# Optimization experiments

Measured on AMD Instinct MI355X. Metric: run time of the kernel, lower is better.

Reference implementation:

```python
import jax, jax.numpy as jnp
import numpy as np

B, N, F_IN, F_E, H, L = 8, 128, 64, 16, 256, 8
EPS = 1e-5


def _linear_params(key, fan_in, fan_out):
    k1, k2 = jax.random.split(key)
    bound = 1.0 / np.sqrt(fan_in)
    W = jax.random.uniform(k1, (fan_in, fan_out), minval=-bound, maxval=bound, dtype=jnp.float32)
    b = jax.random.uniform(k2, (fan_out,), minval=-bound, maxval=bound, dtype=jnp.float32)
    return W, b


def setup_inputs() -> dict:
    key = jax.random.key(0)
    ks = jax.random.split(key, 16)
    x = jax.random.normal(ks[0], (B, N, F_IN), dtype=jnp.float32)
    adj = jax.random.randint(ks[1], (B, N, N), 0, 2, dtype=jnp.int32)
    edge_attr = jax.random.normal(ks[2], (B, N, N, F_E), dtype=jnp.float32)
    mask = jnp.ones((B, N), dtype=jnp.int32)

    node_W, node_b = _linear_params(ks[3], F_IN, H)
    edge_W, edge_b = _linear_params(ks[4], F_E, H)

    lks = jax.random.split(ks[5], L)
    W1s, b1s, W2s, b2s = [], [], [], []
    for i in range(L):
        a, b_ = jax.random.split(lks[i])
        W1, b1 = _linear_params(a, H, H)
        W2, b2 = _linear_params(b_, H, H)
        W1s.append(W1); b1s.append(b1); W2s.append(W2); b2s.append(b2)
    ln_g = jnp.ones((L, H), dtype=jnp.float32)
    ln_b = jnp.zeros((L, H), dtype=jnp.float32)
    W1 = jnp.stack(W1s); b1 = jnp.stack(b1s)
    W2 = jnp.stack(W2s); b2 = jnp.stack(b2s)

    ro_pW, ro_pb = _linear_params(ks[6], H, H)
    ro_aW, ro_ab = _linear_params(ks[7], H, 1)
    ph_W, ph_b = _linear_params(ks[8], H, 1)

    return dict(x=x, adj=adj, edge_attr=edge_attr, mask=mask,
                node_W=node_W, node_b=node_b, edge_W=edge_W, edge_b=edge_b,
                ln_g=ln_g, ln_b=ln_b, W1=W1, b1=b1, W2=W2, b2=b2,
                ro_pW=ro_pW, ro_pb=ro_pb, ro_aW=ro_aW, ro_ab=ro_ab,
                ph_W=ph_W, ph_b=ph_b)


def _layernorm(x, g, b):
    mu = jnp.mean(x, axis=-1, keepdims=True)
    var = jnp.var(x, axis=-1, keepdims=True)
    return (x - mu) * jax.lax.rsqrt(var + EPS) * g + b


def _gine_forward(x, adjf, edge_attr, maskf,
                  node_W, node_b, edge_W, edge_b,
                  ln_g, ln_b, W1, b1, W2, b2,
                  ro_pW, ro_pb, ro_aW, ro_ab, ph_W, ph_b):
    h = x @ node_W + node_b                      # (B,N,H)
    edge_emb = edge_attr @ edge_W + edge_b       # (B,N,N,H)
    m = maskf[..., None]                         # (B,N,1)

    def layer(h, p):
        g, bln, w1, bb1, w2, bb2 = p
        h = h * m
        h_norm = _layernorm(h, g, bln)
        # message: h_j + e_ij, j indexes axis 2 -> broadcast over axis 1
        m_in = h_norm[:, None, :, :] + edge_emb          # (B,N,N,H)
        mm = jax.nn.relu(jax.nn.relu(m_in @ w1 + bb1) @ w2 + bb2)
        mm = mm * adjf[..., None]
        msg = mm.sum(axis=2)                             # (B,N,H)
        out = (h + msg) * m
        return out, None

    h, _ = jax.lax.scan(layer, h, (ln_g, ln_b, W1, b1, W2, b2))

    # attention readout
    hp = jnp.tanh(h @ ro_pW + ro_pb)
    scores = (hp @ ro_aW).squeeze(-1) + ro_ab            # (B,N)
    scores = jnp.where(maskf > 0, scores, -jnp.inf)
    alpha = jax.nn.softmax(scores, axis=1)
    cnt = jnp.clip(maskf.sum(axis=1, keepdims=True), 1.0, None)
    fallback = jnp.where(maskf > 0, 1.0 / cnt, 0.0)
    alpha = jnp.where(jnp.isnan(alpha), fallback, alpha)
    gvec = (h * alpha[..., None]).sum(axis=1)            # (B,H)
    out = (gvec @ ph_W + ph_b).squeeze(-1)               # (B,)
    return out


def reference(x, adj, edge_attr, mask,
              node_W, node_b, edge_W, edge_b,
              ln_g, ln_b, W1, b1, W2, b2,
              ro_pW, ro_pb, ro_aW, ro_ab, ph_W, ph_b):
    adjf = adj.astype(jnp.float32)
    maskf = mask.astype(jnp.float32)
    return _gine_forward(x, adjf, edge_attr, maskf,
                         node_W, node_b, edge_W, edge_b,
                         ln_g, ln_b, W1, b1, W2, b2,
                         ro_pW, ro_pb, ro_aW, ro_ab, ph_W, ph_b)
```

## Files before the change

kernel.cpp:

```cpp
#include <hip/hip_runtime.h>

typedef float  f32x4   __attribute__((ext_vector_type(4)));
typedef short  bf16x8  __attribute__((ext_vector_type(8)));
typedef unsigned short u16;
typedef unsigned int   u32;

static __device__ __forceinline__ u16 f2bf(float f) {
    u32 u = __float_as_uint(f);
    u += 0x7FFFu + ((u >> 16) & 1u);
    return (u16)(u >> 16);
}



__global__ void k_h0ln(const float* __restrict__ x, const float* __restrict__ nW,
                       const float* __restrict__ nb, const int* __restrict__ mask,
                       const float* __restrict__ lng, const float* __restrict__ lnb,
                       float* __restrict__ h, u16* __restrict__ hnbf) {
    __shared__ float xr[64];
    __shared__ float rs[4], rs2[4];
    int row = blockIdx.x, c = threadIdx.x;
    if (c < 64) xr[c] = x[row * 64 + c];
    __syncthreads();
    float acc = nb[c];
#pragma unroll
    for (int k = 0; k < 64; ++k) acc += xr[k] * nW[k * 256 + c];
    float mv = (float)mask[row];
    float v = acc * mv;
    h[row * 256 + c] = v;
    float s = v, s2 = v * v;
    int w = c >> 6, lane = c & 63;
#pragma unroll
    for (int off = 32; off; off >>= 1) {
        s  += __shfl_xor(s,  off);
        s2 += __shfl_xor(s2, off);
    }
    if (lane == 0) { rs[w] = s; rs2[w] = s2; }
    __syncthreads();
    float S  = rs[0] + rs[1] + rs[2] + rs[3];
    float S2 = rs2[0] + rs2[1] + rs2[2] + rs2[3];
    float mu  = S * (1.f / 256.f);
    float var = S2 * (1.f / 256.f) - mu * mu;
    float rstd = rsqrtf(var + 1e-5f);
    hnbf[row * 256 + c] = f2bf((v - mu) * rstd * lng[c] + lnb[c]);
}

__global__ void k_edgefrag(const float* __restrict__ ea, u16* __restrict__ ef) {
    int gid = blockIdx.x * 256 + threadIdx.x;
    int lane = gid & 63, nt = (gid >> 6) & 7, i = (gid >> 9) & 127, b = gid >> 16;
    int j = nt * 16 + (lane & 15), k0 = (lane >> 4) * 8;
    uint4 out = {0u, 0u, 0u, 0u};
    if (k0 < 16) {
        const float* p = ea + (((size_t)(b * 128 + i) * 128 + j) * 16 + k0);
        u16 us[8];
#pragma unroll
        for (int t = 0; t < 8; ++t) us[t] = f2bf(p[t]);
        out.x = (u32)us[0] | ((u32)us[1] << 16);
        out.y = (u32)us[2] | ((u32)us[3] << 16);
        out.z = (u32)us[4] | ((u32)us[5] << 16);
        out.w = (u32)us[6] | ((u32)us[7] << 16);
    }
    ((uint4*)ef)[gid] = out;
}

__global__ void k_wt(const float* __restrict__ W1, const float* __restrict__ W2,
                     u16* __restrict__ w1t, u16* __restrict__ w2t) {
    int gid = blockIdx.x * 256 + threadIdx.x;
    int lane = gid & 63, mt = (gid >> 6) & 15, kt = (gid >> 10) & 7, l = gid >> 13;
    int hh = mt * 16 + (lane & 15), k = kt * 32 + (lane >> 4) * 8;
    u16 a[8], b[8];
#pragma unroll
    for (int t = 0; t < 8; ++t) {
        size_t idx = (size_t)l * 65536 + (size_t)(k + t) * 256 + hh;
        a[t] = f2bf(W1[idx]);
        b[t] = f2bf(W2[idx]);
    }
    uint4 oa, ob;
    oa.x = (u32)a[0] | ((u32)a[1] << 16); oa.y = (u32)a[2] | ((u32)a[3] << 16);
    oa.z = (u32)a[4] | ((u32)a[5] << 16); oa.w = (u32)a[6] | ((u32)a[7] << 16);
    ob.x = (u32)b[0] | ((u32)b[1] << 16); ob.y = (u32)b[2] | ((u32)b[3] << 16);
    ob.z = (u32)b[4] | ((u32)b[5] << 16); ob.w = (u32)b[6] | ((u32)b[7] << 16);
    ((uint4*)w1t)[gid] = oa;
    ((uint4*)w2t)[gid] = ob;
}

__global__ void k_pwt(const float* __restrict__ pW, u16* __restrict__ pwt) {
    int gid = blockIdx.x * 256 + threadIdx.x;
    int lane = gid & 63, mt = (gid >> 6) & 15, kt = gid >> 10;
    int hh = mt * 16 + (lane & 15), k = kt * 32 + (lane >> 4) * 8;
    u16 a[8];
#pragma unroll
    for (int t = 0; t < 8; ++t) a[t] = f2bf(pW[(size_t)(k + t) * 256 + hh]);
    uint4 o;
    o.x = (u32)a[0] | ((u32)a[1] << 16); o.y = (u32)a[2] | ((u32)a[3] << 16);
    o.z = (u32)a[4] | ((u32)a[5] << 16); o.w = (u32)a[6] | ((u32)a[7] << 16);
    ((uint4*)pwt)[gid] = o;
}

__global__ void k_wf1b(const float* __restrict__ eW, const float* __restrict__ eb,
                       const float* __restrict__ W1, const float* __restrict__ b1,
                       u16* __restrict__ wf, float* __restrict__ bias1) {
    __shared__ float eWsT[256 * 16];
    __shared__ float ebS[256];
    int l = blockIdx.x, tid = threadIdx.x;
#pragma unroll
    for (int k = 0; k < 16; ++k) eWsT[tid * 16 + k] = eW[k * 256 + tid];
    ebS[tid] = eb[tid];
    __syncthreads();
    float acc[16];
#pragma unroll
    for (int k = 0; k < 16; ++k) acc[k] = 0.f;
    float bacc = b1[l * 256 + tid];
    const float* w1c = W1 + (size_t)l * 65536 + tid;
    for (int c = 0; c < 256; ++c) {
        float wv = w1c[(size_t)c * 256];
        const f32x4* e = (const f32x4*)&eWsT[c * 16];
#pragma unroll
        for (int q = 0; q < 4; ++q) {
            f32x4 ev = e[q];
#pragma unroll
            for (int t = 0; t < 4; ++t) acc[q * 4 + t] += ev[t] * wv;
        }
        bacc += ebS[c] * wv;
    }
    bias1[l * 256 + tid] = bacc;
    int mt = tid >> 4, lo = tid & 15;
#pragma unroll
    for (int c4 = 0; c4 < 4; ++c4) {
        u16 us[8];
#pragma unroll
        for (int t = 0; t < 8; ++t) {
            int k = c4 * 8 + t;
            us[t] = (k < 16) ? f2bf(acc[k]) : (u16)0;
        }
        uint4 o;
        o.x = (u32)us[0] | ((u32)us[1] << 16);
        o.y = (u32)us[2] | ((u32)us[3] << 16);
        o.z = (u32)us[4] | ((u32)us[5] << 16);
        o.w = (u32)us[6] | ((u32)us[7] << 16);
        ((uint4*)wf)[(size_t)(l * 16 + mt) * 64 + c4 * 16 + lo] = o;
    }
}


__global__ __launch_bounds__(256) void k_hn1(const u16* __restrict__ w1t,
        const u16* __restrict__ hnbf, const float* __restrict__ bias1,
        float* __restrict__ hn1p, int l) {
    int orig = blockIdx.x;
    int bid = (orig & 7) * 16 + (orig >> 3);
    int b = bid >> 4, mt = bid & 15;
    int tid = threadIdx.x, w = tid >> 6, lane = tid & 63;
    f32x4 bv = *(const f32x4*)(bias1 + l * 256 + mt * 16 + (lane >> 4) * 4);
    f32x4 acc0 = bv, acc1 = bv;
    int j0 = (w * 2) * 16 + (lane & 15), j1 = j0 + 16;
#pragma unroll
    for (int kt = 0; kt < 8; ++kt) {
        bf16x8 a = *(const bf16x8*)(w1t + ((size_t)((l * 8 + kt) * 16 + mt) * 64 + lane) * 8);
        bf16x8 bt0 = *(const bf16x8*)(hnbf + ((size_t)(b * 128 + j0) * 256 + kt * 32 + (lane >> 4) * 8));
        bf16x8 bt1 = *(const bf16x8*)(hnbf + ((size_t)(b * 128 + j1) * 256 + kt * 32 + (lane >> 4) * 8));
        acc0 = __builtin_amdgcn_mfma_f32_16x16x32_bf16(a, bt0, acc0, 0, 0, 0);
        acc1 = __builtin_amdgcn_mfma_f32_16x16x32_bf16(a, bt1, acc1, 0, 0, 0);
    }
    float* outb = hn1p + (size_t)b * 32768;
    *(f32x4*)(outb + ((size_t)(mt * 8 + w * 2) * 64 + lane) * 4)     = acc0;
    *(f32x4*)(outb + ((size_t)(mt * 8 + w * 2 + 1) * 64 + lane) * 4) = acc1;
}

__global__ __launch_bounds__(512, 4) void k_msg(
        const u16* __restrict__ wf1t, const u16* __restrict__ ef,
        const u16* __restrict__ w2t,  const float* __restrict__ hn1p,
        const float* __restrict__ b2, const int* __restrict__ adj,
        const int* __restrict__ mask, float* __restrict__ h,
        const float* __restrict__ lngN, const float* __restrict__ lnbN,
        u16* __restrict__ hnbf, int l, int doLN) {

    __shared__ __align__(16) u16  t1S[8 * 8 * 64 * 8];
    __shared__ __align__(16) float b2S[256];
    __shared__ __align__(16) float msgS[256];
    __shared__ int rankS[128];
    __shared__ int cntS;
    __shared__ float rs[8], rs2[8];

    int orig = blockIdx.x;
    int bid = (orig & 7) * 128 + (orig >> 3);
    int b = bid >> 7, i = bid & 127;
    int tid = threadIdx.x, w = tid >> 6, lane = tid & 63;
    int row = b * 128 + i;

    if (tid < 256) b2S[tid] = b2[l * 256 + tid];
    if (w == 0) {
        int f0 = adj[(size_t)row * 128 + lane] != 0;
        int f1 = adj[(size_t)row * 128 + 64 + lane] != 0;
        unsigned long long m0 = __ballot(f0);
        unsigned long long m1 = __ballot(f1);
        unsigned long long lt = (1ull << lane) - 1ull;
        int c0 = __popcll(m0);
        rankS[lane]      = f0 ? __popcll(m0 & lt)      : -1;
        rankS[64 + lane] = f1 ? c0 + __popcll(m1 & lt) : -1;
        if (lane == 0) cntS = c0 + __popcll(m1);
    }
    __syncthreads();
    int cnt = cntS;
    int NT = (cnt + 15) >> 4;

    {
        int c = cnt + (lane >> 2);
        int kg = lane & 3;
        if (c < NT * 16) {
            uint4 z = {0u, 0u, 0u, 0u};
            *(uint4*)(t1S + ((size_t)((w * 8 + (c >> 4)) * 64 + kg * 16 + (c & 15)) * 8)) = z;
        }
    }

    const u16*  efb = ef + (size_t)row * 4096;
    const float* hpb = hn1p + (size_t)b * 32768;
    int mt0 = w * 2, mt1 = w * 2 + 1;
    bf16x8 aG0 = *(const bf16x8*)(wf1t + ((size_t)(l * 16 + mt0) * 64 + lane) * 8);
    bf16x8 aG1 = *(const bf16x8*)(wf1t + ((size_t)(l * 16 + mt1) * 64 + lane) * 8);
    int g0   = (lane >> 5) * 16;
    int g1   = 32 + g0;
    int toff = ((lane >> 4) & 1) * 4;
#pragma unroll
    for (int nt = 0; nt < 8; ++nt) {
        bf16x8 be = *(const bf16x8*)(efb + (size_t)(nt * 64 + lane) * 8);
        int r = rankS[nt * 16 + (lane & 15)];
        f32x4 ci0 = *(const f32x4*)(hpb + ((size_t)(mt0 * 8 + nt) * 64 + lane) * 4);
        f32x4 acc0 = __builtin_amdgcn_mfma_f32_16x16x32_bf16(aG0, be, ci0, 0, 0, 0);
        f32x4 ci1 = *(const f32x4*)(hpb + ((size_t)(mt1 * 8 + nt) * 64 + lane) * 4);
        f32x4 acc1 = __builtin_amdgcn_mfma_f32_16x16x32_bf16(aG1, be, ci1, 0, 0, 0);
        if (r >= 0) {
            int base = (w * 8 + (r >> 4)) * 64 + (r & 15);
            uint2 pk0, pk1;
            pk0.x = (u32)f2bf(fmaxf(acc0[0], 0.f)) | ((u32)f2bf(fmaxf(acc0[1], 0.f)) << 16);
            pk0.y = (u32)f2bf(fmaxf(acc0[2], 0.f)) | ((u32)f2bf(fmaxf(acc0[3], 0.f)) << 16);
            pk1.x = (u32)f2bf(fmaxf(acc1[0], 0.f)) | ((u32)f2bf(fmaxf(acc1[1], 0.f)) << 16);
            pk1.y = (u32)f2bf(fmaxf(acc1[2], 0.f)) | ((u32)f2bf(fmaxf(acc1[3], 0.f)) << 16);
            *(uint2*)(t1S + ((size_t)(base + g0)) * 8 + toff) = pk0;
            *(uint2*)(t1S + ((size_t)(base + g1)) * 8 + toff) = pk1;
        }
    }
    __syncthreads();

    bf16x8 a2[8][2];
#pragma unroll
    for (int kt = 0; kt < 8; ++kt) {
        a2[kt][0] = *(const bf16x8*)(w2t + ((size_t)((l * 8 + kt) * 16 + mt0) * 64 + lane) * 8);
        a2[kt][1] = *(const bf16x8*)(w2t + ((size_t)((l * 8 + kt) * 16 + mt1) * 64 + lane) * 8);
    }
    int hb0 = mt0 * 16 + (lane >> 4) * 4;
    int hb1 = mt1 * 16 + (lane >> 4) * 4;
    f32x4 bv0 = *(const f32x4*)(&b2S[hb0]);
    f32x4 bv1 = *(const f32x4*)(&b2S[hb1]);
    f32x4 ms0 = (f32x4){0.f, 0.f, 0.f, 0.f};
    f32x4 ms1 = (f32x4){0.f, 0.f, 0.f, 0.f};
    for (int n = 0; n < NT; ++n) {
        f32x4 acc0 = (f32x4){0.f, 0.f, 0.f, 0.f};
        f32x4 acc1 = (f32x4){0.f, 0.f, 0.f, 0.f};
#pragma unroll
        for (int kt = 0; kt < 8; ++kt) {
            bf16x8 bt = *(const bf16x8*)(t1S + ((size_t)(kt * 8 + n) * 64 + lane) * 8);
            acc0 = __builtin_amdgcn_mfma_f32_16x16x32_bf16(a2[kt][0], bt, acc0, 0, 0, 0);
            acc1 = __builtin_amdgcn_mfma_f32_16x16x32_bf16(a2[kt][1], bt, acc1, 0, 0, 0);
        }
        bool ok = (n * 16 + (lane & 15)) < cnt;
#pragma unroll
        for (int r = 0; r < 4; ++r) {
            ms0[r] += ok ? fmaxf(acc0[r] + bv0[r], 0.f) : 0.f;
            ms1[r] += ok ? fmaxf(acc1[r] + bv1[r], 0.f) : 0.f;
        }
    }
#pragma unroll
    for (int r = 0; r < 4; ++r) {
        ms0[r] += __shfl_xor(ms0[r], 1); ms1[r] += __shfl_xor(ms1[r], 1);
        ms0[r] += __shfl_xor(ms0[r], 2); ms1[r] += __shfl_xor(ms1[r], 2);
        ms0[r] += __shfl_xor(ms0[r], 4); ms1[r] += __shfl_xor(ms1[r], 4);
        ms0[r] += __shfl_xor(ms0[r], 8); ms1[r] += __shfl_xor(ms1[r], 8);
    }
    if ((lane & 15) == 0) {
        *(f32x4*)(&msgS[hb0]) = ms0;
        *(f32x4*)(&msgS[hb1]) = ms1;
    }
    __syncthreads();

    float v = 0.f;
    if (tid < 256) {
        float mv = (float)mask[row];
        v = (h[(size_t)row * 256 + tid] + msgS[tid]) * mv;
        h[(size_t)row * 256 + tid] = v;
    }
    float s = v, s2 = v * v;
#pragma unroll
    for (int off = 32; off; off >>= 1) {
        s  += __shfl_xor(s,  off);
        s2 += __shfl_xor(s2, off);
    }
    if (lane == 0) { rs[w] = s; rs2[w] = s2; }
    __syncthreads();
    if (tid < 256) {
        float o;
        if (doLN) {
            float S = 0.f, S2 = 0.f;
#pragma unroll
            for (int t = 0; t < 8; ++t) { S += rs[t]; S2 += rs2[t]; }
            float mu  = S * (1.f / 256.f);
            float var = S2 * (1.f / 256.f) - mu * mu;
            float rstd = rsqrtf(var + 1e-5f);
            o = (v - mu) * rstd * lngN[tid] + lnbN[tid];
        } else o = v;
        hnbf[(size_t)row * 256 + tid] = f2bf(o);
    }
}


__global__ __launch_bounds__(512) void k_ro1(const u16* __restrict__ hbf,
        const u16* __restrict__ pwt, const float* __restrict__ pb,
        const float* __restrict__ aW, const float* __restrict__ ab,
        float* __restrict__ scores) {
    int b = blockIdx.x;
    int tid = threadIdx.x, w = tid >> 6, lane = tid & 63;
    f32x4 acc[16];
#pragma unroll
    for (int mt = 0; mt < 16; ++mt)
        acc[mt] = *(const f32x4*)(pb + mt * 16 + (lane >> 4) * 4);
#pragma unroll
    for (int kt = 0; kt < 8; ++kt) {
        bf16x8 bt = *(const bf16x8*)(hbf + ((size_t)(b * 128 + w * 16 + (lane & 15)) * 256 + kt * 32 + (lane >> 4) * 8));
#pragma unroll
        for (int mt = 0; mt < 16; ++mt) {
            bf16x8 a = *(const bf16x8*)(pwt + ((size_t)(kt * 16 + mt) * 64 + lane) * 8);
            acc[mt] = __builtin_amdgcn_mfma_f32_16x16x32_bf16(a, bt, acc[mt], 0, 0, 0);
        }
    }
    float sc = 0.f;
#pragma unroll
    for (int mt = 0; mt < 16; ++mt) {
#pragma unroll
        for (int r = 0; r < 4; ++r)
            sc += tanhf(acc[mt][r]) * aW[mt * 16 + (lane >> 4) * 4 + r];
    }
    sc += __shfl_xor(sc, 16);
    sc += __shfl_xor(sc, 32);
    if (lane < 16) scores[b * 128 + w * 16 + lane] = sc + ab[0];
}

__global__ void k_ro2(const float* __restrict__ h, const float* __restrict__ scores,
                      const int* __restrict__ mask, const float* __restrict__ phW,
                      const float* __restrict__ phb, float* __restrict__ out) {
    __shared__ float aS[128];
    __shared__ float rm[4], rc[4], red[4];
    int b = blockIdx.x, tid = threadIdx.x, w = tid >> 6, lane = tid & 63;
    float mv = 0.f, sv = -__builtin_inff();
    if (tid < 128) {
        mv = (float)mask[b * 128 + tid];
        if (mv > 0.f) sv = scores[b * 128 + tid];
    }
    float mx = sv, cs = mv;
#pragma unroll
    for (int off = 32; off; off >>= 1) {
        mx = fmaxf(mx, __shfl_xor(mx, off));
        cs += __shfl_xor(cs, off);
    }
    if (lane == 0) { rm[w] = mx; rc[w] = cs; }
    __syncthreads();
    mx = fmaxf(fmaxf(rm[0], rm[1]), fmaxf(rm[2], rm[3]));
    float cnt = rc[0] + rc[1] + rc[2] + rc[3];
    float e = (tid < 128 && mv > 0.f) ? expf(sv - mx) : 0.f;
    float se = e;
#pragma unroll
    for (int off = 32; off; off >>= 1) se += __shfl_xor(se, off);
    if (lane == 0) red[w] = se;
    __syncthreads();
    float S = red[0] + red[1] + red[2] + red[3];
    if (tid < 128) {
        float a;
        if (S > 0.f) a = e / S;
        else         a = (mv > 0.f) ? 1.f / fmaxf(cnt, 1.f) : 0.f;
        aS[tid] = a;
    }
    __syncthreads();
    float g = 0.f;
    const float* hb = h + (size_t)b * 128 * 256;
    for (int n = 0; n < 128; ++n) g += aS[n] * hb[(size_t)n * 256 + tid];
    float p = g * phW[tid];
#pragma unroll
    for (int off = 32; off; off >>= 1) p += __shfl_xor(p, off);
    __syncthreads();
    if (lane == 0) red[w] = p;
    __syncthreads();
    if (tid == 0) out[b] = red[0] + red[1] + red[2] + red[3] + phb[0];
}

extern "C" void kernel_launch(void* const* d_in, const int* in_sizes, int n_in,
                              void* d_out, int out_size, void* d_ws, size_t ws_size,
                              hipStream_t stream) {
    const float* x    = (const float*)d_in[0];
    const int*   adj  = (const int*)  d_in[1];
    const float* ea   = (const float*)d_in[2];
    const int*   mask = (const int*)  d_in[3];
    const float* nW   = (const float*)d_in[4];
    const float* nb   = (const float*)d_in[5];
    const float* eW   = (const float*)d_in[6];
    const float* eb   = (const float*)d_in[7];
    const float* lng  = (const float*)d_in[8];
    const float* lnb  = (const float*)d_in[9];
    const float* W1   = (const float*)d_in[10];
    const float* b1   = (const float*)d_in[11];
    const float* W2   = (const float*)d_in[12];
    const float* b2   = (const float*)d_in[13];
    const float* ropW = (const float*)d_in[14];
    const float* ropb = (const float*)d_in[15];
    const float* roaW = (const float*)d_in[16];
    const float* roab = (const float*)d_in[17];
    const float* phW  = (const float*)d_in[18];
    const float* phb  = (const float*)d_in[19];
    float* out = (float*)d_out;

    char* p = (char*)d_ws;
    auto alloc = [&](size_t bytes) { char* r = p; p += (bytes + 255) & ~(size_t)255; return r; };
    float* h     = (float*)alloc((size_t)8 * 128 * 256 * 4);
    u16*   hnbf  = (u16*)  alloc((size_t)8 * 128 * 256 * 2);
    float* hn1p  = (float*)alloc((size_t)8 * 32768 * 4);
    u16*   ef    = (u16*)  alloc((size_t)8 * 128 * 4096 * 2);
    u16*   wf1t  = (u16*)  alloc((size_t)8 * 16 * 64 * 8 * 2);
    u16*   w1t   = (u16*)  alloc((size_t)8 * 8 * 16 * 64 * 8 * 2);
    u16*   w2t   = (u16*)  alloc((size_t)8 * 8 * 16 * 64 * 8 * 2);
    u16*   pwt   = (u16*)  alloc((size_t)8 * 16 * 64 * 8 * 2);
    float* bias1 = (float*)alloc((size_t)8 * 256 * 4);
    float* scores= (float*)alloc((size_t)1024 * 4);

    k_h0ln    <<<1024, 256, 0, stream>>>(x, nW, nb, mask, lng, lnb, h, hnbf);
    k_edgefrag<<<2048, 256, 0, stream>>>(ea, ef);
    k_wt      <<<256,  256, 0, stream>>>(W1, W2, w1t, w2t);
    k_wf1b    <<<8,    256, 0, stream>>>(eW, eb, W1, b1, wf1t, bias1);
    k_pwt     <<<32,   256, 0, stream>>>(ropW, pwt);

    for (int l = 0; l < 8; ++l) {
        k_hn1<<<128,  256, 0, stream>>>(w1t, hnbf, bias1, hn1p, l);
        int doLN = (l < 7) ? 1 : 0;
        int ln_next = (l < 7) ? (l + 1) : l;
        k_msg<<<1024, 512, 0, stream>>>(wf1t, ef, w2t, hn1p, b2, adj, mask, h,
                                        lng + ln_next * 256, lnb + ln_next * 256,
                                        hnbf, l, doLN);
    }

    k_ro1<<<8,   512, 0, stream>>>(hnbf, pwt, ropb, roaW, roab, scores);
    k_ro2<<<8,   256, 0, stream>>>(h, scores, mask, phW, phb, out);
}
```

Before: 377.2 us.

## Process two node rows per k_msg block and store hn1 partials as bf16

Each k_msg block now handles two destination rows of the same graph instead of one. The W2 fragments are loaded into registers once and reused for both rows, and the second row's layer-norm tail is interleaved with the next row's GEMM, so the grid is halved. The hn1p intermediate written by k_hn1 is now stored as packed bf16 and unpacked in k_msg, which halves its memory traffic but adds rounding error to the pre-activation. Fewer blocks and more serial work per block could reduce latency hiding.

```diff
diff --git a/kernel.cpp b/kernel.cpp
--- a/kernel.cpp
+++ b/kernel.cpp
@@ -9,6 +9,14 @@
     u32 u = __float_as_uint(f);
     u += 0x7FFFu + ((u >> 16) & 1u);
     return (u16)(u >> 16);
+}
+static __device__ __forceinline__ f32x4 unpk(uint2 p) {
+    f32x4 r;
+    r[0] = __uint_as_float(p.x << 16);
+    r[1] = __uint_as_float(p.x & 0xFFFF0000u);
+    r[2] = __uint_as_float(p.y << 16);
+    r[3] = __uint_as_float(p.y & 0xFFFF0000u);
+    return r;
 }
 
 
@@ -145,7 +153,7 @@
 
 __global__ __launch_bounds__(256) void k_hn1(const u16* __restrict__ w1t,
         const u16* __restrict__ hnbf, const float* __restrict__ bias1,
-        float* __restrict__ hn1p, int l) {
+        u16* __restrict__ hn1p, int l) {
     int orig = blockIdx.x;
     int bid = (orig & 7) * 16 + (orig >> 3);
     int b = bid >> 4, mt = bid & 15;
@@ -161,14 +169,19 @@
         acc0 = __builtin_amdgcn_mfma_f32_16x16x32_bf16(a, bt0, acc0, 0, 0, 0);
         acc1 = __builtin_amdgcn_mfma_f32_16x16x32_bf16(a, bt1, acc1, 0, 0, 0);
     }
-    float* outb = hn1p + (size_t)b * 32768;
-    *(f32x4*)(outb + ((size_t)(mt * 8 + w * 2) * 64 + lane) * 4)     = acc0;
-    *(f32x4*)(outb + ((size_t)(mt * 8 + w * 2 + 1) * 64 + lane) * 4) = acc1;
+    u16* outb = hn1p + (size_t)b * 32768;
+    uint2 p0, p1;
+    p0.x = (u32)f2bf(acc0[0]) | ((u32)f2bf(acc0[1]) << 16);
+    p0.y = (u32)f2bf(acc0[2]) | ((u32)f2bf(acc0[3]) << 16);
+    p1.x = (u32)f2bf(acc1[0]) | ((u32)f2bf(acc1[1]) << 16);
+    p1.y = (u32)f2bf(acc1[2]) | ((u32)f2bf(acc1[3]) << 16);
+    *(uint2*)(outb + ((size_t)(mt * 8 + w * 2) * 64 + lane) * 4)     = p0;
+    *(uint2*)(outb + ((size_t)(mt * 8 + w * 2 + 1) * 64 + lane) * 4) = p1;
 }
 
 __global__ __launch_bounds__(512, 4) void k_msg(
         const u16* __restrict__ wf1t, const u16* __restrict__ ef,
-        const u16* __restrict__ w2t,  const float* __restrict__ hn1p,
+        const u16* __restrict__ w2t,  const u16* __restrict__ hn1p,
         const float* __restrict__ b2, const int* __restrict__ adj,
         const int* __restrict__ mask, float* __restrict__ h,
         const float* __restrict__ lngN, const float* __restrict__ lnbN,
@@ -177,138 +190,168 @@
     __shared__ __align__(16) u16  t1S[8 * 8 * 64 * 8];
     __shared__ __align__(16) float b2S[256];
     __shared__ __align__(16) float msgS[256];
-    __shared__ int rankS[128];
-    __shared__ int cntS;
+    __shared__ int rankS[2][128];
+    __shared__ int cntS[2];
     __shared__ float rs[8], rs2[8];
 
     int orig = blockIdx.x;
-    int bid = (orig & 7) * 128 + (orig >> 3);
-    int b = bid >> 7, i = bid & 127;
+    int bid = (orig & 7) * 64 + (orig >> 3);
+    int b = bid >> 6, ip = bid & 63;
+    int i0 = ip * 2;
     int tid = threadIdx.x, w = tid >> 6, lane = tid & 63;
-    int row = b * 128 + i;
+    int row0 = b * 128 + i0;
 
     if (tid < 256) b2S[tid] = b2[l * 256 + tid];
-    if (w == 0) {
-        int f0 = adj[(size_t)row * 128 + lane] != 0;
-        int f1 = adj[(size_t)row * 128 + 64 + lane] != 0;
+    if (w < 2) {
+        int rr = row0 + w;
+        int f0 = adj[(size_t)rr * 128 + lane] != 0;
+        int f1 = adj[(size_t)rr * 128 + 64 + lane] != 0;
         unsigned long long m0 = __ballot(f0);
         unsigned long long m1 = __ballot(f1);
         unsigned long long lt = (1ull << lane) - 1ull;
         int c0 = __popcll(m0);
-        rankS[lane]      = f0 ? __popcll(m0 & lt)      : -1;
-        rankS[64 + lane] = f1 ? c0 + __popcll(m1 & lt) : -1;
-        if (lane == 0) cntS = c0 + __popcll(m1);
-    }
-    __syncthreads();
-    int cnt = cntS;
-    int NT = (cnt + 15) >> 4;
-
-    {
-        int c = cnt + (lane >> 2);
-        int kg = lane & 3;
-        if (c < NT * 16) {
-            uint4 z = {0u, 0u, 0u, 0u};
-            *(uint4*)(t1S + ((size_t)((w * 8 + (c >> 4)) * 64 + kg * 16 + (c & 15)) * 8)) = z;
-        }
-    }
-
-    const u16*  efb = ef + (size_t)row * 4096;
-    const float* hpb = hn1p + (size_t)b * 32768;
+        rankS[w][lane]      = f0 ? __popcll(m0 & lt)      : -1;
+        rankS[w][64 + lane] = f1 ? c0 + __popcll(m1 & lt) : -1;
+        if (lane == 0) cntS[w] = c0 + __popcll(m1);
+    }
+    __syncthreads();
+
     int mt0 = w * 2, mt1 = w * 2 + 1;
+    bf16x8 a2[8][2];
+#pragma unroll
+    for (int kt = 0; kt < 8; ++kt) {
+        a2[kt][0] = *(const bf16x8*)(w2t + ((size_t)((l * 8 + kt) * 16 + mt0) * 64 + lane) * 8);
+        a2[kt][1] = *(const bf16x8*)(w2t + ((size_t)((l * 8 + kt) * 16 + mt1) * 64 + lane) * 8);
+    }
     bf16x8 aG0 = *(const bf16x8*)(wf1t + ((size_t)(l * 16 + mt0) * 64 + lane) * 8);
     bf16x8 aG1 = *(const bf16x8*)(wf1t + ((size_t)(l * 16 + mt1) * 64 + lane) * 8);
+
+    const u16* hpb = hn1p + (size_t)b * 32768;
     int g0   = (lane >> 5) * 16;
     int g1   = 32 + g0;
     int toff = ((lane >> 4) & 1) * 4;
-#pragma unroll
-    for (int nt = 0; nt < 8; ++nt) {
-        bf16x8 be = *(const bf16x8*)(efb + (size_t)(nt * 64 + lane) * 8);
-        int r = rankS[nt * 16 + (lane & 15)];
-        f32x4 ci0 = *(const f32x4*)(hpb + ((size_t)(mt0 * 8 + nt) * 64 + lane) * 4);
-        f32x4 acc0 = __builtin_amdgcn_mfma_f32_16x16x32_bf16(aG0, be, ci0, 0, 0, 0);
-        f32x4 ci1 = *(const f32x4*)(hpb + ((size_t)(mt1 * 8 + nt) * 64 + lane) * 4);
-        f32x4 acc1 = __builtin_amdgcn_mfma_f32_16x16x32_bf16(aG1, be, ci1, 0, 0, 0);
-        if (r >= 0) {
-            int base = (w * 8 + (r >> 4)) * 64 + (r & 15);
-            uint2 pk0, pk1;
-            pk0.x = (u32)f2bf(fmaxf(acc0[0], 0.f)) | ((u32)f2bf(fmaxf(acc0[1], 0.f)) << 16);
-            pk0.y = (u32)f2bf(fmaxf(acc0[2], 0.f)) | ((u32)f2bf(fmaxf(acc0[3], 0.f)) << 16);
-            pk1.x = (u32)f2bf(fmaxf(acc1[0], 0.f)) | ((u32)f2bf(fmaxf(acc1[1], 0.f)) << 16);
-            pk1.y = (u32)f2bf(fmaxf(acc1[2], 0.f)) | ((u32)f2bf(fmaxf(acc1[3], 0.f)) << 16);
-            *(uint2*)(t1S + ((size_t)(base + g0)) * 8 + toff) = pk0;
-            *(uint2*)(t1S + ((size_t)(base + g1)) * 8 + toff) = pk1;
-        }
-    }
-    __syncthreads();
-
-    bf16x8 a2[8][2];
-#pragma unroll
-    for (int kt = 0; kt < 8; ++kt) {
-        a2[kt][0] = *(const bf16x8*)(w2t + ((size_t)((l * 8 + kt) * 16 + mt0) * 64 + lane) * 8);
-        a2[kt][1] = *(const bf16x8*)(w2t + ((size_t)((l * 8 + kt) * 16 + mt1) * 64 + lane) * 8);
-    }
     int hb0 = mt0 * 16 + (lane >> 4) * 4;
     int hb1 = mt1 * 16 + (lane >> 4) * 4;
     f32x4 bv0 = *(const f32x4*)(&b2S[hb0]);
     f32x4 bv1 = *(const f32x4*)(&b2S[hb1]);
-    f32x4 ms0 = (f32x4){0.f, 0.f, 0.f, 0.f};
-    f32x4 ms1 = (f32x4){0.f, 0.f, 0.f, 0.f};
-    for (int n = 0; n < NT; ++n) {
-        f32x4 acc0 = (f32x4){0.f, 0.f, 0.f, 0.f};
-        f32x4 acc1 = (f32x4){0.f, 0.f, 0.f, 0.f};
-#pragma unroll
-        for (int kt = 0; kt < 8; ++kt) {
-            bf16x8 bt = *(const bf16x8*)(t1S + ((size_t)(kt * 8 + n) * 64 + lane) * 8);
-            acc0 = __builtin_amdgcn_mfma_f32_16x16x32_bf16(a2[kt][0], bt, acc0, 0, 0, 0);
-            acc1 = __builtin_amdgcn_mfma_f32_16x16x32_bf16(a2[kt][1], bt, acc1, 0, 0, 0);
-        }
-        bool ok = (n * 16 + (lane & 15)) < cnt;
-#pragma unroll
-        for (int r = 0; r < 4; ++r) {
-            ms0[r] += ok ? fmaxf(acc0[r] + bv0[r], 0.f) : 0.f;
-            ms1[r] += ok ? fmaxf(acc1[r] + bv1[r], 0.f) : 0.f;
-        }
-    }
-#pragma unroll
-    for (int r = 0; r < 4; ++r) {
-        ms0[r] += __shfl_xor(ms0[r], 1); ms1[r] += __shfl_xor(ms1[r], 1);
-        ms0[r] += __shfl_xor(ms0[r], 2); ms1[r] += __shfl_xor(ms1[r], 2);
-        ms0[r] += __shfl_xor(ms0[r], 4); ms1[r] += __shfl_xor(ms1[r], 4);
-        ms0[r] += __shfl_xor(ms0[r], 8); ms1[r] += __shfl_xor(ms1[r], 8);
-    }
-    if ((lane & 15) == 0) {
-        *(f32x4*)(&msgS[hb0]) = ms0;
-        *(f32x4*)(&msgS[hb1]) = ms1;
-    }
-    __syncthreads();
-
-    float v = 0.f;
-    if (tid < 256) {
-        float mv = (float)mask[row];
-        v = (h[(size_t)row * 256 + tid] + msgS[tid]) * mv;
-        h[(size_t)row * 256 + tid] = v;
-    }
-    float s = v, s2 = v * v;
-#pragma unroll
-    for (int off = 32; off; off >>= 1) {
-        s  += __shfl_xor(s,  off);
-        s2 += __shfl_xor(s2, off);
-    }
-    if (lane == 0) { rs[w] = s; rs2[w] = s2; }
-    __syncthreads();
-    if (tid < 256) {
-        float o;
-        if (doLN) {
-            float S = 0.f, S2 = 0.f;
-#pragma unroll
-            for (int t = 0; t < 8; ++t) { S += rs[t]; S2 += rs2[t]; }
-            float mu  = S * (1.f / 256.f);
-            float var = S2 * (1.f / 256.f) - mu * mu;
-            float rstd = rsqrtf(var + 1e-5f);
-            o = (v - mu) * rstd * lngN[tid] + lnbN[tid];
-        } else o = v;
-        hnbf[(size_t)row * 256 + tid] = f2bf(o);
-    }
+
+    float vkeep = 0.f;
+    int rowc = row0;
+
+#define ZEROTAIL(CNT, NTv)                                                        \
+    {   int c = (CNT) + (lane >> 2); int kg = lane & 3;                           \
+        if (c < (NTv) * 16) {                                                     \
+            uint4 z = {0u, 0u, 0u, 0u};                                           \
+            *(uint4*)(t1S + ((size_t)((w * 8 + (c >> 4)) * 64 + kg * 16 + (c & 15)) * 8)) = z; } }
+
+#define GEMM1(ROW, II)                                                            \
+    {   const u16* efb = ef + (size_t)(ROW) * 4096;                               \
+        _Pragma("unroll")                                                         \
+        for (int nt = 0; nt < 8; ++nt) {                                          \
+            bf16x8 be = *(const bf16x8*)(efb + (size_t)(nt * 64 + lane) * 8);     \
+            int r = rankS[II][nt * 16 + (lane & 15)];                             \
+            uint2 c0p = *(const uint2*)(hpb + ((size_t)(mt0 * 8 + nt) * 64 + lane) * 4); \
+            f32x4 acc0 = __builtin_amdgcn_mfma_f32_16x16x32_bf16(aG0, be, unpk(c0p), 0, 0, 0); \
+            uint2 c1p = *(const uint2*)(hpb + ((size_t)(mt1 * 8 + nt) * 64 + lane) * 4); \
+            f32x4 acc1 = __builtin_amdgcn_mfma_f32_16x16x32_bf16(aG1, be, unpk(c1p), 0, 0, 0); \
+            if (r >= 0) {                                                         \
+                int base = (w * 8 + (r >> 4)) * 64 + (r & 15);                    \
+                uint2 pk0, pk1;                                                   \
+                pk0.x = (u32)f2bf(fmaxf(acc0[0], 0.f)) | ((u32)f2bf(fmaxf(acc0[1], 0.f)) << 16); \
+                pk0.y = (u32)f2bf(fmaxf(acc0[2], 0.f)) | ((u32)f2bf(fmaxf(acc0[3], 0.f)) << 16); \
+                pk1.x = (u32)f2bf(fmaxf(acc1[0], 0.f)) | ((u32)f2bf(fmaxf(acc1[1], 0.f)) << 16); \
+                pk1.y = (u32)f2bf(fmaxf(acc1[2], 0.f)) | ((u32)f2bf(fmaxf(acc1[3], 0.f)) << 16); \
+                *(uint2*)(t1S + ((size_t)(base + g0)) * 8 + toff) = pk0;          \
+                *(uint2*)(t1S + ((size_t)(base + g1)) * 8 + toff) = pk1;          \
+            } } }
+
+#define GEMM2RED(CNT)                                                             \
+    {   int NTv = ((CNT) + 15) >> 4;                                              \
+        f32x4 ms0 = (f32x4){0.f, 0.f, 0.f, 0.f};                                  \
+        f32x4 ms1 = (f32x4){0.f, 0.f, 0.f, 0.f};                                  \
+        for (int n = 0; n < NTv; ++n) {                                           \
+            f32x4 acc0 = (f32x4){0.f, 0.f, 0.f, 0.f};                             \
+            f32x4 acc1 = (f32x4){0.f, 0.f, 0.f, 0.f};                             \
+            _Pragma("unroll")                                                     \
+            for (int kt = 0; kt < 8; ++kt) {                                      \
+                bf16x8 bt = *(const bf16x8*)(t1S + ((size_t)(kt * 8 + n) * 64 + lane) * 8); \
+                acc0 = __builtin_amdgcn_mfma_f32_16x16x32_bf16(a2[kt][0], bt, acc0, 0, 0, 0); \
+                acc1 = __builtin_amdgcn_mfma_f32_16x16x32_bf16(a2[kt][1], bt, acc1, 0, 0, 0); \
+            }                                                                     \
+            bool ok = (n * 16 + (lane & 15)) < (CNT);                             \
+            _Pragma("unroll")                                                     \
+            for (int r = 0; r < 4; ++r) {                                         \
+                ms0[r] += ok ? fmaxf(acc0[r] + bv0[r], 0.f) : 0.f;                \
+                ms1[r] += ok ? fmaxf(acc1[r] + bv1[r], 0.f) : 0.f;                \
+            } }                                                                   \
+        _Pragma("unroll")                                                         \
+        for (int r = 0; r < 4; ++r) {                                             \
+            ms0[r] += __shfl_xor(ms0[r], 1); ms1[r] += __shfl_xor(ms1[r], 1);     \
+            ms0[r] += __shfl_xor(ms0[r], 2); ms1[r] += __shfl_xor(ms1[r], 2);     \
+            ms0[r] += __shfl_xor(ms0[r], 4); ms1[r] += __shfl_xor(ms1[r], 4);     \
+            ms0[r] += __shfl_xor(ms0[r], 8); ms1[r] += __shfl_xor(ms1[r], 8);     \
+        }                                                                         \
+        if ((lane & 15) == 0) {                                                   \
+            *(f32x4*)(&msgS[hb0]) = ms0;                                          \
+            *(f32x4*)(&msgS[hb1]) = ms1;                                          \
+        } }
+
+#define TAIL_A(ROW)                                                               \
+    {   vkeep = 0.f;                                                              \
+        if (tid < 256) {                                                          \
+            float mv = (float)mask[ROW];                                          \
+            vkeep = (h[(size_t)(ROW) * 256 + tid] + msgS[tid]) * mv;              \
+            h[(size_t)(ROW) * 256 + tid] = vkeep;                                 \
+        }                                                                         \
+        float s = vkeep, s2 = vkeep * vkeep;                                      \
+        _Pragma("unroll")                                                         \
+        for (int off = 32; off; off >>= 1) {                                      \
+            s  += __shfl_xor(s,  off);                                            \
+            s2 += __shfl_xor(s2, off);                                            \
+        }                                                                         \
+        if (lane == 0) { rs[w] = s; rs2[w] = s2; } }
+
+#define TAIL_B(ROW)                                                               \
+    if (tid < 256) {                                                              \
+        float o;                                                                  \
+        if (doLN) {                                                               \
+            float S = 0.f, S2 = 0.f;                                              \
+            _Pragma("unroll")                                                     \
+            for (int t = 0; t < 8; ++t) { S += rs[t]; S2 += rs2[t]; }             \
+            float mu  = S * (1.f / 256.f);                                        \
+            float var = S2 * (1.f / 256.f) - mu * mu;                             \
+            float rstd = rsqrtf(var + 1e-5f);                                     \
+            o = (vkeep - mu) * rstd * lngN[tid] + lnbN[tid];                      \
+        } else o = vkeep;                                                         \
+        hnbf[(size_t)(ROW) * 256 + tid] = f2bf(o);                                \
+    }
+
+    int cnt0 = cntS[0], cnt1 = cntS[1];
+    int NT0 = (cnt0 + 15) >> 4, NT1 = (cnt1 + 15) >> 4;
+
+    ZEROTAIL(cnt0, NT0);
+    GEMM1(row0, 0);
+    __syncthreads();
+    GEMM2RED(cnt0);
+    __syncthreads();
+    rowc = row0;
+    TAIL_A(rowc);
+    ZEROTAIL(cnt1, NT1);
+    GEMM1(row0 + 1, 1);
+    __syncthreads();
+    TAIL_B(rowc);
+    GEMM2RED(cnt1);
+    __syncthreads();
+    rowc = row0 + 1;
+    TAIL_A(rowc);
+    __syncthreads();
+    TAIL_B(rowc);
+
+#undef ZEROTAIL
+#undef GEMM1
+#undef GEMM2RED
+#undef TAIL_A
+#undef TAIL_B
 }
 
 
@@ -419,7 +462,7 @@
     auto alloc = [&](size_t bytes) { char* r = p; p += (bytes + 255) & ~(size_t)255; return r; };
     float* h     = (float*)alloc((size_t)8 * 128 * 256 * 4);
     u16*   hnbf  = (u16*)  alloc((size_t)8 * 128 * 256 * 2);
-    float* hn1p  = (float*)alloc((size_t)8 * 32768 * 4);
+    u16*   hn1p  = (u16*)  alloc((size_t)8 * 32768 * 2);
     u16*   ef    = (u16*)  alloc((size_t)8 * 128 * 4096 * 2);
     u16*   wf1t  = (u16*)  alloc((size_t)8 * 16 * 64 * 8 * 2);
     u16*   w1t   = (u16*)  alloc((size_t)8 * 8 * 16 * 64 * 8 * 2);
@@ -438,9 +481,9 @@
         k_hn1<<<128,  256, 0, stream>>>(w1t, hnbf, bias1, hn1p, l);
         int doLN = (l < 7) ? 1 : 0;
         int ln_next = (l < 7) ? (l + 1) : l;
-        k_msg<<<1024, 512, 0, stream>>>(wf1t, ef, w2t, hn1p, b2, adj, mask, h,
-                                        lng + ln_next * 256, lnb + ln_next * 256,
-                                        hnbf, l, doLN);
+        k_msg<<<512, 512, 0, stream>>>(wf1t, ef, w2t, hn1p, b2, adj, mask, h,
+                                       lng + ln_next * 256, lnb + ln_next * 256,
+                                       hnbf, l, doLN);
     }
 
     k_ro1<<<8,   512, 0, stream>>>(hnbf, pwt, ropb, roaW, roab, scores);
```

After: 417.5 us. 1.11x slower.
